# Kernel optimization log

Hardware: AMD Instinct MI355X
Metric: run time of the kernel (lower is better)

## Reference

```python
import jax, jax.numpy as jnp
import numpy as np

ENT_TYPES = 9
INNER_DIM = 64


def setup_inputs() -> dict:
    key = jax.random.key(0)
    k1, k2 = jax.random.split(key)
    B, S, H = 8, 1024, 768
    last_hidden_state = jax.random.normal(k1, (B, S, H), dtype=jnp.float32)
    attention_mask = jnp.ones((B, S), dtype=jnp.float32)
    dense_w = jax.random.normal(k2, (ENT_TYPES * INNER_DIM * 2, H), dtype=jnp.float32) * (1.0 / np.sqrt(H))
    dense_b = jnp.zeros((ENT_TYPES * INNER_DIM * 2,), dtype=jnp.float32)
    return {
        "last_hidden_state": last_hidden_state,
        "attention_mask": attention_mask,
        "dense_w": dense_w,
        "dense_b": dense_b,
    }


def _sinusoidal_pos_emb(seq_len: int, output_dim: int, dtype):
    # (seq_len, output_dim) interleaved as [sin0, cos0, sin1, cos1, ...]
    position = jnp.arange(seq_len, dtype=dtype)[:, None]              # (S, 1)
    indices = jnp.arange(output_dim // 2, dtype=dtype)
    inv_freq = jnp.power(jnp.asarray(10000.0, dtype), -2.0 * indices / output_dim)
    ang = position * inv_freq                                         # (S, D/2)
    emb = jnp.stack([jnp.sin(ang), jnp.cos(ang)], axis=-1)            # (S, D/2, 2)
    return emb.reshape(seq_len, output_dim)


def reference(last_hidden_state, attention_mask, dense_w, dense_b):
    B, S, H = last_hidden_state.shape
    D = INNER_DIM
    E = ENT_TYPES

    # dense projection then split into per-entity-type q/k of width D each
    out = last_hidden_state @ dense_w.T + dense_b                     # (B, S, 2*E*D)
    out = out.reshape(B, S, E, 2 * D)                                 # (B, S, E, 2D)
    qw, kw = out[..., :D], out[..., D:]                               # (B, S, E, D)

    # RoPE: duplicated cos/sin pairs, half-rotation
    pos = _sinusoidal_pos_emb(S, D, last_hidden_state.dtype)          # (S, D)
    cos_pos = jnp.repeat(pos[:, 1::2], 2, axis=-1)[None, :, None, :]  # (1, S, 1, D)
    sin_pos = jnp.repeat(pos[:, 0::2], 2, axis=-1)[None, :, None, :]

    def rotate_half(x):
        x1, x2 = x[..., : D // 2], x[..., D // 2 :]
        return jnp.concatenate([-x2, x1], axis=-1)

    qw = qw * cos_pos + rotate_half(qw) * sin_pos
    kw = kw * cos_pos + rotate_half(kw) * sin_pos

    # pairwise entity scores
    logits = jnp.einsum("bmhd,bnhd->bhmn", qw, kw) / jnp.sqrt(jnp.asarray(D, logits_dtype := last_hidden_state.dtype))

    # padding mask along key axis (as in original)
    pad_mask = attention_mask[:, None, None, :]                       # (B, 1, 1, S)
    logits = logits * pad_mask - (1.0 - pad_mask) * 10000.0

    # upper-triangular validity mask (start <= end)
    tri = jnp.triu(jnp.ones((S, S), dtype=logits.dtype))[None, None]  # (1, 1, S, S)
    logits = logits - (1.0 - tri) * 10000.0
    return logits
```

## Files before the change

### kernel.cpp

```cpp
#include <hip/hip_runtime.h>

#define BB 8
#define SS 1024
#define HH 768
#define EE 9
#define DD 64
#define NCOL (EE * 2 * DD)

typedef __bf16 bf16x8 __attribute__((ext_vector_type(8)));
typedef float f32x4 __attribute__((ext_vector_type(4)));

__device__ __forceinline__ unsigned short f2b(float f) {
    unsigned int x = __float_as_uint(f);
    unsigned int r = (x + 0x7fffu + ((x >> 16) & 1u)) >> 16;
    return (unsigned short)r;
}

#define LDA1 40
__global__ __launch_bounds__(256) void dense_rope_mfma(
    const float* __restrict__ lhs,
    const float* __restrict__ W,
    const float* __restrict__ bias,
    unsigned short* __restrict__ q_ws,
    unsigned short* __restrict__ k_ws) {
    __shared__ unsigned short As[128 * LDA1];
    __shared__ unsigned short Bs[128 * LDA1];

    const int t = threadIdx.x;
    const int lane = t & 63, wave = t >> 6;
    const int quad = lane >> 4, lr = lane & 15;
    const int wm = wave >> 1, wn = wave & 1;
    const int j0 = blockIdx.x * 128;
    const int m0 = blockIdx.y * 128;

    f32x4 acc[4][4] = {};

    for (int kt = 0; kt < HH / 32; ++kt) {
        const int k0 = kt * 32;
        float4 av[4], bv[4];
#pragma unroll
        for (int i = 0; i < 4; ++i) {
            int idx = t + i * 256;
            int row = idx >> 3, c4 = (idx & 7) * 4;
            av[i] = *(const float4*)&lhs[(size_t)(m0 + row) * HH + k0 + c4];
            bv[i] = *(const float4*)&W[(size_t)(j0 + row) * HH + k0 + c4];
        }
        __syncthreads();
#pragma unroll
        for (int i = 0; i < 4; ++i) {
            int idx = t + i * 256;
            int row = idx >> 3, c4 = (idx & 7) * 4;
            ushort4 a4 = {f2b(av[i].x), f2b(av[i].y), f2b(av[i].z), f2b(av[i].w)};
            ushort4 b4 = {f2b(bv[i].x), f2b(bv[i].y), f2b(bv[i].z), f2b(bv[i].w)};
            *(ushort4*)&As[row * LDA1 + c4] = a4;
            *(ushort4*)&Bs[row * LDA1 + c4] = b4;
        }
        __syncthreads();

        bf16x8 af[4], bf[4];
#pragma unroll
        for (int mt = 0; mt < 4; ++mt)
            af[mt] = *(const bf16x8*)&As[(wm * 64 + mt * 16 + lr) * LDA1 + quad * 8];
#pragma unroll
        for (int nt = 0; nt < 4; ++nt)
            bf[nt] = *(const bf16x8*)&Bs[(wn * 64 + nt * 16 + lr) * LDA1 + quad * 8];
#pragma unroll
        for (int mt = 0; mt < 4; ++mt)
#pragma unroll
            for (int nt = 0; nt < 4; ++nt)
                acc[mt][nt] = __builtin_amdgcn_mfma_f32_16x16x32_bf16(
                    af[mt], bf[nt], acc[mt][nt], 0, 0, 0);
    }

    const int gcol0 = j0 + wn * 64;
    const int g = gcol0 >> 6;
    const int e = g >> 1;
    unsigned short* dst = (g & 1) ? k_ws : q_ws;
    const int b_idx = m0 >> 10;
    const size_t zbase = (size_t)(b_idx * EE + e) * SS;
    const float L2_1E4_D32 = 0.4152410118609203f;

    float bb[4], invf[4];
#pragma unroll
    for (int nt = 0; nt < 4; ++nt) {
        bb[nt] = bias[gcol0 + nt * 16 + lr];
        int half = (nt * 16 + lr) >> 1;
        invf[nt] = exp2f(-(float)half * L2_1E4_D32);
    }
    const int s0 = (m0 & (SS - 1)) + wm * 64;
#pragma unroll
    for (int mt = 0; mt < 4; ++mt) {
#pragma unroll
        for (int reg = 0; reg < 4; ++reg) {
            const int s = s0 + mt * 16 + quad * 4 + reg;
            float c[4];
#pragma unroll
            for (int nt = 0; nt < 4; ++nt) c[nt] = acc[mt][nt][reg] + bb[nt];
#pragma unroll
            for (int nt = 0; nt < 4; ++nt) {
                float rot = (nt < 2) ? -c[nt + 2] : c[nt - 2];
                float ang = (float)s * invf[nt];
                float sv, cv;
                __sincosf(ang, &sv, &cv);
                const int d = nt * 16 + lr;
                dst[(zbase + s) * DD + d] = f2b(c[nt] * cv + rot * sv);
            }
        }
    }
}

#define LDA2 72
__global__ __launch_bounds__(256) void logits_mfma(
    const unsigned short* __restrict__ q_ws,
    const unsigned short* __restrict__ k_ws,
    const float* __restrict__ mask,
    float* __restrict__ out) {
    __shared__ unsigned short Qs[128 * LDA2];
    __shared__ unsigned short Ks[128 * LDA2];

    const int t = threadIdx.x;
    const int lane = t & 63, wave = t >> 6;
    const int quad = lane >> 4, lr = lane & 15;
    const int wm = wave >> 1, wn = wave & 1;
    const int n0 = blockIdx.x * 128;
    const int m0 = blockIdx.y * 128;
    const int z = blockIdx.z;
    const int b_idx = z / EE;

    const uint4* qsrc = (const uint4*)(q_ws + ((size_t)z * SS + m0) * DD);
    const uint4* ksrc = (const uint4*)(k_ws + ((size_t)z * SS + n0) * DD);
#pragma unroll
    for (int i = 0; i < 4; ++i) {
        int idx = t + i * 256;
        int row = idx >> 3, c8 = (idx & 7) * 8;
        uint4 qv = qsrc[idx];
        uint4 kv = ksrc[idx];
        *(uint4*)&Qs[row * LDA2 + c8] = qv;
        *(uint4*)&Ks[row * LDA2 + c8] = kv;
    }
    __syncthreads();

    f32x4 acc[4][4] = {};
#pragma unroll
    for (int ks = 0; ks < DD; ks += 32) {
        bf16x8 af[4], bf[4];
#pragma unroll
        for (int mt = 0; mt < 4; ++mt)
            af[mt] = *(const bf16x8*)&Qs[(wm * 64 + mt * 16 + lr) * LDA2 + ks + quad * 8];
#pragma unroll
        for (int nt = 0; nt < 4; ++nt)
            bf[nt] = *(const bf16x8*)&Ks[(wn * 64 + nt * 16 + lr) * LDA2 + ks + quad * 8];
#pragma unroll
        for (int mt = 0; mt < 4; ++mt)
#pragma unroll
            for (int nt = 0; nt < 4; ++nt)
                acc[mt][nt] = __builtin_amdgcn_mfma_f32_16x16x32_bf16(
                    af[mt], bf[nt], acc[mt][nt], 0, 0, 0);
    }

    float p[4];
#pragma unroll
    for (int nt = 0; nt < 4; ++nt)
        p[nt] = mask[b_idx * SS + n0 + wn * 64 + nt * 16 + lr];

    float* outz = out + (size_t)z * SS * SS;
#pragma unroll
    for (int mt = 0; mt < 4; ++mt) {
#pragma unroll
        for (int reg = 0; reg < 4; ++reg) {
            const int m = m0 + wm * 64 + mt * 16 + quad * 4 + reg;
#pragma unroll
            for (int nt = 0; nt < 4; ++nt) {
                const int n = n0 + wn * 64 + nt * 16 + lr;
                float v = acc[mt][nt][reg] * 0.125f;
                v = v * p[nt] - (1.0f - p[nt]) * 10000.0f;
                if (n < m) v -= 10000.0f;
                outz[(size_t)m * SS + n] = v;
            }
        }
    }
}

extern "C" void kernel_launch(void* const* d_in, const int* in_sizes, int n_in,
                              void* d_out, int out_size, void* d_ws, size_t ws_size,
                              hipStream_t stream) {
    const float* lhs  = (const float*)d_in[0];
    const float* mask = (const float*)d_in[1];
    const float* W    = (const float*)d_in[2];
    const float* bias = (const float*)d_in[3];
    float* out = (float*)d_out;

    unsigned short* q_ws = (unsigned short*)d_ws;
    unsigned short* k_ws = q_ws + (size_t)BB * EE * SS * DD;

    dim3 g1(NCOL / 128, (BB * SS) / 128);
    dense_rope_mfma<<<g1, 256, 0, stream>>>(lhs, W, bias, q_ws, k_ws);

    dim3 g2(SS / 128, SS / 128, BB * EE);
    logits_mfma<<<g2, 256, 0, stream>>>(q_ws, k_ws, mask, out);
}
```

Measured before the change: 403.7 us.

## Pre-convert GEMM operands to bf16 and stage tiles with direct global-to-LDS loads

Two small kernels now convert the hidden states and the dense weights to bf16 in workspace before the projection runs. The dense+RoPE kernel then fills its shared-memory tiles with global_load_lds 16-byte direct loads instead of loading fp32 into registers, converting, and storing to LDS. This removes the conversion work that was repeated for every column block, and it halves the bytes each GEMM tile load reads. The cost is an extra read/write pass over the inputs and two more launches. The LDS rows also lose their padding, which may cause bank conflicts on the fragment reads.

```diff
diff --git a/kernel.cpp b/kernel.cpp
--- a/kernel.cpp
+++ b/kernel.cpp
@@ -16,15 +16,30 @@
     return (unsigned short)r;
 }
 
-#define LDA1 40
+__device__ __forceinline__ void gload_lds16(const void* g, void* l) {
+    __builtin_amdgcn_global_load_lds(
+        (const __attribute__((address_space(1))) void*)g,
+        (__attribute__((address_space(3))) void*)l, 16, 0, 0);
+}
+
+__global__ __launch_bounds__(256) void to_bf16(const float* __restrict__ in,
+                                               unsigned short* __restrict__ out,
+                                               int n4) {
+    int i = blockIdx.x * 256 + threadIdx.x;
+    if (i >= n4) return;
+    float4 v = ((const float4*)in)[i];
+    ushort4 o = {f2b(v.x), f2b(v.y), f2b(v.z), f2b(v.w)};
+    ((ushort4*)out)[i] = o;
+}
+
 __global__ __launch_bounds__(256) void dense_rope_mfma(
-    const float* __restrict__ lhs,
-    const float* __restrict__ W,
+    const unsigned short* __restrict__ Abf,
+    const unsigned short* __restrict__ Wbf,
     const float* __restrict__ bias,
     unsigned short* __restrict__ q_ws,
     unsigned short* __restrict__ k_ws) {
-    __shared__ unsigned short As[128 * LDA1];
-    __shared__ unsigned short Bs[128 * LDA1];
+    __shared__ unsigned short As[128 * 32];
+    __shared__ unsigned short Bs[128 * 32];
 
     const int t = threadIdx.x;
     const int lane = t & 63, wave = t >> 6;
@@ -35,35 +50,28 @@
 
     f32x4 acc[4][4] = {};
 
+    const int srow = wave * 16 + (lane >> 2);
+    const int sc8 = (lane & 3) * 8;
+
     for (int kt = 0; kt < HH / 32; ++kt) {
         const int k0 = kt * 32;
-        float4 av[4], bv[4];
-#pragma unroll
-        for (int i = 0; i < 4; ++i) {
-            int idx = t + i * 256;
-            int row = idx >> 3, c4 = (idx & 7) * 4;
-            av[i] = *(const float4*)&lhs[(size_t)(m0 + row) * HH + k0 + c4];
-            bv[i] = *(const float4*)&W[(size_t)(j0 + row) * HH + k0 + c4];
+        __syncthreads();
+#pragma unroll
+        for (int i = 0; i < 2; ++i) {
+            const int row = i * 64 + srow;
+            const int lb = i * 2048 + wave * 512;
+            gload_lds16(&Abf[(size_t)(m0 + row) * HH + k0 + sc8], &As[lb]);
+            gload_lds16(&Wbf[(size_t)(j0 + row) * HH + k0 + sc8], &Bs[lb]);
         }
         __syncthreads();
-#pragma unroll
-        for (int i = 0; i < 4; ++i) {
-            int idx = t + i * 256;
-            int row = idx >> 3, c4 = (idx & 7) * 4;
-            ushort4 a4 = {f2b(av[i].x), f2b(av[i].y), f2b(av[i].z), f2b(av[i].w)};
-            ushort4 b4 = {f2b(bv[i].x), f2b(bv[i].y), f2b(bv[i].z), f2b(bv[i].w)};
-            *(ushort4*)&As[row * LDA1 + c4] = a4;
-            *(ushort4*)&Bs[row * LDA1 + c4] = b4;
-        }
-        __syncthreads();
 
         bf16x8 af[4], bf[4];
 #pragma unroll
         for (int mt = 0; mt < 4; ++mt)
-            af[mt] = *(const bf16x8*)&As[(wm * 64 + mt * 16 + lr) * LDA1 + quad * 8];
+            af[mt] = *(const bf16x8*)&As[(wm * 64 + mt * 16 + lr) * 32 + quad * 8];
 #pragma unroll
         for (int nt = 0; nt < 4; ++nt)
-            bf[nt] = *(const bf16x8*)&Bs[(wn * 64 + nt * 16 + lr) * LDA1 + quad * 8];
+            bf[nt] = *(const bf16x8*)&Bs[(wn * 64 + nt * 16 + lr) * 32 + quad * 8];
 #pragma unroll
         for (int mt = 0; mt < 4; ++mt)
 #pragma unroll
@@ -192,9 +200,14 @@
 
     unsigned short* q_ws = (unsigned short*)d_ws;
     unsigned short* k_ws = q_ws + (size_t)BB * EE * SS * DD;
+    unsigned short* Abf  = k_ws + (size_t)BB * EE * SS * DD;
+    unsigned short* Wbf  = Abf + (size_t)BB * SS * HH;
+
+    to_bf16<<<(BB * SS * HH) / 4 / 256, 256, 0, stream>>>(lhs, Abf, (BB * SS * HH) / 4);
+    to_bf16<<<(NCOL * HH) / 4 / 256, 256, 0, stream>>>(W, Wbf, (NCOL * HH) / 4);
 
     dim3 g1(NCOL / 128, (BB * SS) / 128);
-    dense_rope_mfma<<<g1, 256, 0, stream>>>(lhs, W, bias, q_ws, k_ws);
+    dense_rope_mfma<<<g1, 256, 0, stream>>>(Abf, Wbf, bias, q_ws, k_ws);
 
     dim3 g2(SS / 128, SS / 128, BB * EE);
     logits_mfma<<<g2, 256, 0, stream>>>(q_ws, k_ws, mask, out);
```

Result: faster. 365.3 us (-9.5%).
